# Optimization experiments

Measured on AMD Instinct MI355X. Metric: run time of the kernel, lower is better.

## Reference

```python
import jax, jax.numpy as jnp
import numpy as np

B, K, H, W = 8, 1024, 24, 24
C = H * W            # in_channels = 576
NH = 6               # hardcoded num_heads
HD = C // NH         # 96


def setup_inputs() -> dict:
    key = jax.random.key(0)
    ks = jax.random.split(key, 8)
    s = 1.0 / np.sqrt(C)
    return {
        "input1": jax.random.normal(ks[0], (B, K, H, W), jnp.float32),
        "input2": jax.random.normal(ks[1], (B, K, H, W), jnp.float32),
        "Wq": jax.random.uniform(ks[2], (C, C), jnp.float32, -s, s),
        "bq": jax.random.uniform(ks[3], (C,), jnp.float32, -s, s),
        "Wk": jax.random.uniform(ks[4], (C, C), jnp.float32, -s, s),
        "bk": jax.random.uniform(ks[5], (C,), jnp.float32, -s, s),
        "Wv": jax.random.uniform(ks[6], (C, C), jnp.float32, -s, s),
        "bv": jax.random.uniform(ks[7], (C,), jnp.float32, -s, s),
    }


def reference(input1, input2, Wq, bq, Wk, bk, Wv, bv):
    b, k, h, w = input1.shape
    c = h * w
    x1 = input1.reshape(b, k, c)
    x2 = input2.reshape(b, k, c)
    # torch nn.Linear: y = x @ W^T + b
    q = x1 @ Wq.T + bq                      # [b, k, c]
    kk = x2 @ Wk.T + bk
    v = x2 @ Wv.T + bv
    # torch .view scrambles: [b, k, c] -> [b, NH, c//NH, k] (row-major reshape)
    q = q.reshape(b, NH, c // NH, k)
    kk = kk.reshape(b, NH, c // NH, k)
    v = v.reshape(b, NH, c // NH, k)
    # scores = q^T k over head-dim; NOTE: no 1/sqrt(d) scaling in original
    scores = jnp.einsum('bhdq,bhdk->bhqk', q, kk)   # [b, NH, k, k]
    weights = jax.nn.softmax(scores, axis=-1)
    # context = value @ weights^T -> [b, NH, hd, k]
    ctx = jnp.einsum('bhdk,bhqk->bhdq', v, weights)
    return ctx.reshape(b, k, h, w)
```

## Files before the change

### kernel.cpp

```cpp
#include <hip/hip_runtime.h>
#include <cmath>

#define BATCH 8
#define KDIM  1024
#define CH    576
#define NHEAD 6
#define HDIM  96

typedef _Float16 f16;
typedef f16 f16x4 __attribute__((ext_vector_type(4)));
typedef f16 f16x8 __attribute__((ext_vector_type(8)));
typedef float f32x16 __attribute__((ext_vector_type(16)));
typedef unsigned int u32;

#define PSZ  (BATCH * KDIM * CH)
#define WSZ  (CH * CH)

__device__ inline f32x16 zero16() {
    f32x16 z;
#pragma unroll
    for (int r = 0; r < 16; ++r) z[r] = 0.f;
    return z;
}

__global__ __launch_bounds__(256) void convert_all(
    const float* __restrict__ x1, const float* __restrict__ x2,
    const float* __restrict__ Wq, const float* __restrict__ Wk,
    const float* __restrict__ Wv,
    f16* __restrict__ x1h, f16* __restrict__ x2h, f16* __restrict__ wh)
{
    const int bid = blockIdx.x;
    const int tid = threadIdx.x;

    __shared__ f16 Ws2[192 * 88];

    if (bid < 81) {
        const int z  = bid / 27;
        const int xb = (bid % 27) / 9;
        const int k0 = bid % 9;
        const float* src = (z == 0) ? Wq : (z == 1) ? Wk : Wv;

#pragma unroll
        for (int r = 0; r < 12; ++r) {
            int idx = r * 256 + tid;
            int row = idx >> 4, c4 = idx & 15;
            float4 u = *(const float4*)&src[(size_t)(xb * 192 + row) * CH + k0 * 64 + c4 * 4];
            f16x4 hv;
            hv[0] = (f16)u.x; hv[1] = (f16)u.y; hv[2] = (f16)u.z; hv[3] = (f16)u.w;
            *(f16x4*)&Ws2[row * 88 + c4 * 4] = hv;
        }
        __syncthreads();

        f16* dst = wh + ((size_t)((z * 3 + xb) * 9 + k0) * 24) * 512;
#pragma unroll
        for (int rr = 0; rr < 6; ++rr) {
            int cc = rr * 256 + tid;
            int lc = cc >> 6, lane = cc & 63;
            int ks = lc / 6, rem = lc % 6;
            int hw = rem / 3, nt = rem % 3;
            int n_local = hw * 96 + nt * 32 + (lane & 31);
            int kk = ks * 16 + (lane >> 5) * 8;
            f16x8 v = *(const f16x8*)&Ws2[n_local * 88 + kk];
            *(f16x8*)&dst[(size_t)cc * 8] = v;
        }
    } else {
        int idx = (bid - 81) * 256 + tid;
        const float* src;
        f16* dst;
        if (idx < PSZ / 8) { src = x1; dst = x1h; }
        else {
            idx -= PSZ / 8;
            if (idx >= PSZ / 8) return;
            src = x2; dst = x2h;
        }
        float4 u0 = ((const float4*)src)[2 * idx];
        float4 u1 = ((const float4*)src)[2 * idx + 1];
        f16x8 hv;
        hv[0] = (f16)u0.x; hv[1] = (f16)u0.y; hv[2] = (f16)u0.z; hv[3] = (f16)u0.w;
        hv[4] = (f16)u1.x; hv[5] = (f16)u1.y; hv[6] = (f16)u1.z; hv[7] = (f16)u1.w;
        ((f16x8*)dst)[idx] = hv;
    }
}

__global__ __launch_bounds__(256, 2) void proj_kernel(
    const f16* __restrict__ x1h, const f16* __restrict__ x2h,
    const f16* __restrict__ wh,
    const float* __restrict__ bq, const float* __restrict__ bk,
    const float* __restrict__ bv,
    f16* __restrict__ qf, f16* __restrict__ kf, f16* __restrict__ VF)
{
    const int bid = blockIdx.x;
    const int k8  = bid & 7;
    const int j   = bid >> 3;
    const int xb  = j % 3;
    const int z   = (j / 3) % 3;
    const int y   = k8 + 8 * (j / 9);

    const f16* A      = (z == 0) ? x1h : x2h;
    const float* bias = (z == 0) ? bq : (z == 1) ? bk : bv;

    __shared__ __align__(16) char sm[25600];
    f16* As = (f16*)sm;
    f16* Es = (f16*)sm;

    const int tid = threadIdx.x;
    const int lane = tid & 63, w = tid >> 6;
    const int l31 = lane & 31, half = lane >> 5;
    const int mw = 64 * (w & 1), nh = 96 * (w >> 1);
    const int nBase = xb * 192;
    const int mBase = y * 128;

    int arow[4], ach[4];
#pragma unroll
    for (int r = 0; r < 4; ++r) {
        int idx = r * 256 + tid;
        arow[r] = idx >> 3; ach[r] = idx & 7;
    }

    const f16* Wfrag = wh + ((size_t)(z * 3 + xb) * 216 + (size_t)(w >> 1) * 3) * 512
                          + (size_t)lane * 8;

    f16x8 aP[4];
#pragma unroll
    for (int r = 0; r < 4; ++r)
        aP[r] = *(const f16x8*)&A[(size_t)(mBase + arow[r]) * CH + ach[r] * 8];

    f16x8 wc[12];
#pragma unroll
    for (int ks = 0; ks < 4; ++ks)
#pragma unroll
        for (int nt = 0; nt < 3; ++nt)
            wc[ks * 3 + nt] = *(const f16x8*)&Wfrag[(size_t)(ks * 6 + nt) * 512];

    f32x16 acc[2][3] = {{zero16(), zero16(), zero16()},
                        {zero16(), zero16(), zero16()}};

    for (int k0i = 0; k0i < 9; ++k0i) {
        __syncthreads();
#pragma unroll
        for (int r = 0; r < 4; ++r)
            *(f16x8*)&As[arow[r] * 72 + ach[r] * 8] = aP[r];
        __syncthreads();
        if (k0i + 1 < 9) {
#pragma unroll
            for (int r = 0; r < 4; ++r)
                aP[r] = *(const f16x8*)&A[(size_t)(mBase + arow[r]) * CH + (k0i + 1) * 64 + ach[r] * 8];
        }
#pragma unroll
        for (int ks = 0; ks < 4; ++ks) {
            f16x8 a0 = *(const f16x8*)&As[(mw + l31) * 72 + 16 * ks + 8 * half];
            f16x8 a1 = *(const f16x8*)&As[(mw + 32 + l31) * 72 + 16 * ks + 8 * half];
#pragma unroll
            for (int nt = 0; nt < 3; ++nt) {
                acc[0][nt] = __builtin_amdgcn_mfma_f32_32x32x16_f16(a0, wc[ks * 3 + nt], acc[0][nt], 0, 0, 0);
                acc[1][nt] = __builtin_amdgcn_mfma_f32_32x32x16_f16(a1, wc[ks * 3 + nt], acc[1][nt], 0, 0, 0);
            }
        }
        if (k0i + 1 < 9) {
            const f16* Wn = Wfrag + (size_t)(k0i + 1) * 24 * 512;
#pragma unroll
            for (int ks = 0; ks < 4; ++ks)
#pragma unroll
                for (int nt = 0; nt < 3; ++nt)
                    wc[ks * 3 + nt] = *(const f16x8*)&Wn[(size_t)(ks * 6 + nt) * 512];
        }
    }

    if (z < 2) {
        f16* dst = (z == 0) ? qf : kf;
#pragma unroll
        for (int nt = 0; nt < 3; ++nt) {
            int n = nBase + nh + 32 * nt + l31;
            float bsv = bias[n];
#pragma unroll
            for (int ms = 0; ms < 2; ++ms)
#pragma unroll
                for (int r = 0; r < 16; ++r) {
                    int m = mBase + mw + 32 * ms + (r & 3) + 8 * (r >> 2) + 4 * half;
                    dst[(size_t)m * CH + n] = (f16)(acc[ms][nt][r] + bsv);
                }
        }
    } else {
        const int b      = y >> 3;
        const int kkBase = (y & 7) * 128;
#pragma unroll
        for (int hs = 0; hs < 2; ++hs) {
            __syncthreads();
            if ((w & 1) == hs) {
#pragma unroll
                for (int nt = 0; nt < 3; ++nt) {
                    int nloc = nh + 32 * nt + l31;
                    float bsv = bias[nBase + nloc];
#pragma unroll
                    for (int ms = 0; ms < 2; ++ms)
#pragma unroll
                        for (int r = 0; r < 16; ++r) {
                            int row_l = 32 * ms + (r & 3) + 8 * (r >> 2) + 4 * half;
                            Es[row_l * 200 + nloc] = (f16)(acc[ms][nt][r] + bsv);
                        }
                }
            }
            __syncthreads();
#pragma unroll
            for (int rr = 0; rr < 6; ++rr) {
                int o = rr * 256 + tid;
                int row_l = o / 24, sl = o % 24;
                int f = (kkBase + hs * 64 + row_l) * 576 + nBase + sl * 8;
                int h = f / 98304;
                int rem = f - h * 98304;
                int d = rem >> 10, t = rem & 1023;
                int tt2 = t >> 6, tl = t & 63;
                int c = (tl >> 5) * 384 + ((tl >> 4) & 1) * 192
                      + (d >> 5) * 64 + (d & 31) + 32 * ((tl >> 3) & 1);
                f16x8 v = *(const f16x8*)&Es[row_l * 200 + sl * 8];
                *(f16x8*)&VF[((size_t)((b * NHEAD + h) * 16 + tt2)) * 6144 + (size_t)c * 8] = v;
            }
        }
    }
}

__global__ __launch_bounds__(256) void repack_qk(
    const f16* __restrict__ qf, const f16* __restrict__ kf,
    f16* __restrict__ QF, f16* __restrict__ KF)
{
    const int tt = blockIdx.x;
    const int bh = blockIdx.y;
    const f16* src = blockIdx.z ? kf : qf;
    f16* dst = blockIdx.z ? KF : QF;
    const int tid = threadIdx.x;

    __shared__ f16 Ts[96 * 72];
    const int rowbase = (bh / NHEAD) * CH + (bh % NHEAD) * HDIM;

#pragma unroll
    for (int r = 0; r < 3; ++r) {
        int idx = r * 256 + tid;
        int d = idx >> 3, g = idx & 7;
        *(f16x8*)&Ts[d * 72 + g * 8] =
            *(const f16x8*)&src[(size_t)(rowbase + d) * KDIM + tt * 64 + g * 8];
    }
    __syncthreads();

    f16* dblk = dst + ((size_t)bh * 16 + tt) * 6144;
#pragma unroll
    for (int r = 0; r < 3; ++r) {
        int c = r * 256 + tid;
        int lane = c & 63;
        int ks = (c >> 6) % 6;
        int jg = c / 384;
        int l31 = lane & 31, half = lane >> 5;
        int jl = jg * 32 + l31;
        int d0 = ks * 16 + half * 8;
        f16x8 v;
#pragma unroll
        for (int u = 0; u < 8; ++u) v[u] = Ts[(d0 + u) * 72 + jl];
        *(f16x8*)&dblk[(size_t)c * 8] = v;
    }
}

__global__ __launch_bounds__(256, 3) void attn_kernel(
    const f16* __restrict__ QF, const f16* __restrict__ KF,
    const f16* __restrict__ VF, float* __restrict__ out)
{
    __shared__ __align__(16) char smem[25600];

    const int bh = blockIdx.x;
    const int qt = blockIdx.y;
    const int h  = bh % NHEAD;
    const int b  = bh / NHEAD;

    const int tid = threadIdx.x;
    const int lane = tid & 63, w = tid >> 6;
    const int ih = w & 1, jg = w >> 1;
    const int l31 = lane & 31, half = lane >> 5;
    const int iw = 32 * ih;

    const f16* Qblk  = QF + ((size_t)bh * 16 + qt) * 6144 + (size_t)ih * 3072 + (size_t)lane * 8;
    const f16* Kfrag = KF + (size_t)bh * 16 * 6144 + (size_t)jg * 3072 + (size_t)lane * 8;
    const f16* Vfrag = VF + (size_t)bh * 16 * 6144 + (size_t)jg * 3072 + (size_t)lane * 8;

    f16x8 qfr[6];
#pragma unroll
    for (int ks = 0; ks < 6; ++ks) {
        qfr[ks] = *(const f16x8*)&Qblk[ks * 512];
#pragma unroll
        for (int u = 0; u < 8; ++u)
            qfr[ks][u] = (f16)((float)qfr[ks][u] * 1.44269504f);
    }

    f16x8 kc[6], vc[6];
#pragma unroll
    for (int ks = 0; ks < 6; ++ks)
        kc[ks] = *(const f16x8*)&Kfrag[ks * 512];
#pragma unroll
    for (int kq = 0; kq < 2; ++kq)
#pragma unroll
        for (int t = 0; t < 3; ++t)
            vc[kq * 3 + t] = *(const f16x8*)&Vfrag[kq * 1536 + t * 512];

    float l_run = 0.f;
    f32x16 Oacc[3] = {zero16(), zero16(), zero16()};

    for (int jt = 0; jt < 16; ++jt) {
        f32x16 s0 = zero16();
#pragma unroll
        for (int ks = 0; ks < 6; ++ks)
            s0 = __builtin_amdgcn_mfma_f32_32x32x16_f16(kc[ks], qfr[ks], s0, 0, 0, 0);

        if (jt + 1 < 16) {
            const f16* Kt = Kfrag + (size_t)(jt + 1) * 6144;
#pragma unroll
            for (int ks = 0; ks < 6; ++ks)
                kc[ks] = *(const f16x8*)&Kt[ks * 512];
        }

        f16x4 pq[4];
#pragma unroll
        for (int r = 0; r < 16; ++r) {
            float e = __builtin_amdgcn_exp2f(s0[r] - 26.0f);
            l_run += e;
            pq[r >> 2][r & 3] = (f16)e;
        }

#pragma unroll
        for (int kq = 0; kq < 2; ++kq) {
            union { f16x4 h; u32 u[2]; } snd, rcv, keep;
            keep.h = half ? pq[2 * kq + 1] : pq[2 * kq];
            snd.h  = half ? pq[2 * kq]     : pq[2 * kq + 1];
            rcv.u[0] = __shfl_xor((int)snd.u[0], 32);
            rcv.u[1] = __shfl_xor((int)snd.u[1], 32);
            f16x8 bp;
            if (half == 0) {
#pragma unroll
                for (int v = 0; v < 4; ++v) { bp[v] = keep.h[v]; bp[4 + v] = rcv.h[v]; }
            } else {
#pragma unroll
                for (int v = 0; v < 4; ++v) { bp[v] = rcv.h[v]; bp[4 + v] = keep.h[v]; }
            }
#pragma unroll
            for (int t = 0; t < 3; ++t)
                Oacc[t] = __builtin_amdgcn_mfma_f32_32x32x16_f16(vc[kq * 3 + t], bp, Oacc[t], 0, 0, 0);
        }

        if (jt + 1 < 16) {
            const f16* Vt = Vfrag + (size_t)(jt + 1) * 6144;
#pragma unroll
            for (int kq = 0; kq < 2; ++kq)
#pragma unroll
                for (int t = 0; t < 3; ++t)
                    vc[kq * 3 + t] = *(const f16x8*)&Vt[kq * 1536 + t * 512];
        }
    }

    l_run += __shfl_xor(l_run, 32);

    float* Oscr = (float*)smem;
    float* lScr = (float*)(smem + 25344);
    if (jg == 1) {
        if (half == 0) lScr[iw + l31] = l_run;
        float* od = Oscr + ih * 3168;
#pragma unroll
        for (int t = 0; t < 3; ++t)
#pragma unroll
            for (int r = 0; r < 16; ++r) {
                int d = 32 * t + (r & 3) + 8 * (r >> 2) + 4 * half;
                od[d * 33 + l31] = Oacc[t][r];
            }
    }
    __syncthreads();
    if (jg == 0) {
        float linv = 1.0f / (l_run + lScr[iw + l31]);
        const float* od = Oscr + ih * 3168;
        float* obase = out + ((size_t)b * CH + (size_t)h * HDIM) * KDIM
                           + qt * 64 + iw + l31;
#pragma unroll
        for (int t = 0; t < 3; ++t)
#pragma unroll
            for (int r = 0; r < 16; ++r) {
                int d = 32 * t + (r & 3) + 8 * (r >> 2) + 4 * half;
                obase[(size_t)d * KDIM] =
                    (Oacc[t][r] + od[d * 33 + l31]) * linv;
            }
    }
}

extern "C" void kernel_launch(void* const* d_in, const int* in_sizes, int n_in,
                              void* d_out, int out_size, void* d_ws, size_t ws_size,
                              hipStream_t stream)
{
    const float* x1 = (const float*)d_in[0];
    const float* x2 = (const float*)d_in[1];
    const float* Wq = (const float*)d_in[2];
    const float* bq = (const float*)d_in[3];
    const float* Wk = (const float*)d_in[4];
    const float* bk = (const float*)d_in[5];
    const float* Wv = (const float*)d_in[6];
    const float* bv = (const float*)d_in[7];
    float* out = (float*)d_out;

    const size_t P = PSZ;
    f16* x1h = (f16*)d_ws;
    f16* x2h = x1h + P;
    f16* qf  = x2h + P;
    f16* kf  = qf + P;
    f16* QF  = kf + P;
    f16* KF  = QF + P;
    f16* VF  = KF + P;
    f16* wh  = VF + P;

    const int xblocks = 2 * (PSZ / 8) / 256;
    convert_all<<<81 + xblocks, 256, 0, stream>>>(x1, x2, Wq, Wk, Wv, x1h, x2h, wh);

    proj_kernel<<<576, 256, 0, stream>>>(x1h, x2h, wh, bq, bk, bv, qf, kf, VF);

    dim3 rgrid(KDIM / 64, BATCH * NHEAD, 2);
    repack_qk<<<rgrid, 256, 0, stream>>>(qf, kf, QF, KF);

    dim3 agrid(BATCH * NHEAD, KDIM / 64);
    attn_kernel<<<agrid, 256, 0, stream>>>(QF, KF, VF, out);
}
```

Baseline: 160.0 us.

## Fuse all stages into one persistent kernel with grid-wide atomic barriers

Replaces the four separate launches (convert, projection, repack, attention) with a single persistent kernel of 512 blocks. Each phase loops over virtual block indices, and phases are separated by a software grid barrier built on an atomic counter, which is reset by a memset before launch. The goal is to remove launch overhead and inter-kernel gaps. In exchange it adds spin-wait barriers, caps attention occupancy at the projection's launch bounds, and risks deadlock if all 512 blocks cannot be co-resident.

```diff
diff --git a/kernel.cpp b/kernel.cpp
--- a/kernel.cpp
+++ b/kernel.cpp
@@ -23,364 +23,372 @@
     return z;
 }
 
-__global__ __launch_bounds__(256) void convert_all(
-    const float* __restrict__ x1, const float* __restrict__ x2,
-    const float* __restrict__ Wq, const float* __restrict__ Wk,
-    const float* __restrict__ Wv,
-    f16* __restrict__ x1h, f16* __restrict__ x2h, f16* __restrict__ wh)
-{
-    const int bid = blockIdx.x;
-    const int tid = threadIdx.x;
-
-    __shared__ f16 Ws2[192 * 88];
-
-    if (bid < 81) {
-        const int z  = bid / 27;
-        const int xb = (bid % 27) / 9;
-        const int k0 = bid % 9;
-        const float* src = (z == 0) ? Wq : (z == 1) ? Wk : Wv;
-
-#pragma unroll
-        for (int r = 0; r < 12; ++r) {
-            int idx = r * 256 + tid;
-            int row = idx >> 4, c4 = idx & 15;
-            float4 u = *(const float4*)&src[(size_t)(xb * 192 + row) * CH + k0 * 64 + c4 * 4];
-            f16x4 hv;
-            hv[0] = (f16)u.x; hv[1] = (f16)u.y; hv[2] = (f16)u.z; hv[3] = (f16)u.w;
-            *(f16x4*)&Ws2[row * 88 + c4 * 4] = hv;
-        }
-        __syncthreads();
-
-        f16* dst = wh + ((size_t)((z * 3 + xb) * 9 + k0) * 24) * 512;
-#pragma unroll
-        for (int rr = 0; rr < 6; ++rr) {
-            int cc = rr * 256 + tid;
-            int lc = cc >> 6, lane = cc & 63;
-            int ks = lc / 6, rem = lc % 6;
-            int hw = rem / 3, nt = rem % 3;
-            int n_local = hw * 96 + nt * 32 + (lane & 31);
-            int kk = ks * 16 + (lane >> 5) * 8;
-            f16x8 v = *(const f16x8*)&Ws2[n_local * 88 + kk];
-            *(f16x8*)&dst[(size_t)cc * 8] = v;
-        }
-    } else {
-        int idx = (bid - 81) * 256 + tid;
-        const float* src;
-        f16* dst;
-        if (idx < PSZ / 8) { src = x1; dst = x1h; }
-        else {
-            idx -= PSZ / 8;
-            if (idx >= PSZ / 8) return;
-            src = x2; dst = x2h;
-        }
-        float4 u0 = ((const float4*)src)[2 * idx];
-        float4 u1 = ((const float4*)src)[2 * idx + 1];
-        f16x8 hv;
-        hv[0] = (f16)u0.x; hv[1] = (f16)u0.y; hv[2] = (f16)u0.z; hv[3] = (f16)u0.w;
-        hv[4] = (f16)u1.x; hv[5] = (f16)u1.y; hv[6] = (f16)u1.z; hv[7] = (f16)u1.w;
-        ((f16x8*)dst)[idx] = hv;
-    }
-}
-
-__global__ __launch_bounds__(256, 2) void proj_kernel(
-    const f16* __restrict__ x1h, const f16* __restrict__ x2h,
-    const f16* __restrict__ wh,
-    const float* __restrict__ bq, const float* __restrict__ bk,
-    const float* __restrict__ bv,
-    f16* __restrict__ qf, f16* __restrict__ kf, f16* __restrict__ VF)
-{
-    const int bid = blockIdx.x;
-    const int k8  = bid & 7;
-    const int j   = bid >> 3;
-    const int xb  = j % 3;
-    const int z   = (j / 3) % 3;
-    const int y   = k8 + 8 * (j / 9);
-
-    const f16* A      = (z == 0) ? x1h : x2h;
-    const float* bias = (z == 0) ? bq : (z == 1) ? bk : bv;
-
-    __shared__ __align__(16) char sm[25600];
-    f16* As = (f16*)sm;
-    f16* Es = (f16*)sm;
-
-    const int tid = threadIdx.x;
-    const int lane = tid & 63, w = tid >> 6;
-    const int l31 = lane & 31, half = lane >> 5;
-    const int mw = 64 * (w & 1), nh = 96 * (w >> 1);
-    const int nBase = xb * 192;
-    const int mBase = y * 128;
-
-    int arow[4], ach[4];
-#pragma unroll
-    for (int r = 0; r < 4; ++r) {
-        int idx = r * 256 + tid;
-        arow[r] = idx >> 3; ach[r] = idx & 7;
-    }
-
-    const f16* Wfrag = wh + ((size_t)(z * 3 + xb) * 216 + (size_t)(w >> 1) * 3) * 512
-                          + (size_t)lane * 8;
-
-    f16x8 aP[4];
-#pragma unroll
-    for (int r = 0; r < 4; ++r)
-        aP[r] = *(const f16x8*)&A[(size_t)(mBase + arow[r]) * CH + ach[r] * 8];
-
-    f16x8 wc[12];
-#pragma unroll
-    for (int ks = 0; ks < 4; ++ks)
-#pragma unroll
-        for (int nt = 0; nt < 3; ++nt)
-            wc[ks * 3 + nt] = *(const f16x8*)&Wfrag[(size_t)(ks * 6 + nt) * 512];
-
-    f32x16 acc[2][3] = {{zero16(), zero16(), zero16()},
-                        {zero16(), zero16(), zero16()}};
-
-    for (int k0i = 0; k0i < 9; ++k0i) {
-        __syncthreads();
-#pragma unroll
-        for (int r = 0; r < 4; ++r)
-            *(f16x8*)&As[arow[r] * 72 + ach[r] * 8] = aP[r];
-        __syncthreads();
-        if (k0i + 1 < 9) {
-#pragma unroll
-            for (int r = 0; r < 4; ++r)
-                aP[r] = *(const f16x8*)&A[(size_t)(mBase + arow[r]) * CH + (k0i + 1) * 64 + ach[r] * 8];
-        }
-#pragma unroll
-        for (int ks = 0; ks < 4; ++ks) {
-            f16x8 a0 = *(const f16x8*)&As[(mw + l31) * 72 + 16 * ks + 8 * half];
-            f16x8 a1 = *(const f16x8*)&As[(mw + 32 + l31) * 72 + 16 * ks + 8 * half];
-#pragma unroll
-            for (int nt = 0; nt < 3; ++nt) {
-                acc[0][nt] = __builtin_amdgcn_mfma_f32_32x32x16_f16(a0, wc[ks * 3 + nt], acc[0][nt], 0, 0, 0);
-                acc[1][nt] = __builtin_amdgcn_mfma_f32_32x32x16_f16(a1, wc[ks * 3 + nt], acc[1][nt], 0, 0, 0);
-            }
-        }
-        if (k0i + 1 < 9) {
-            const f16* Wn = Wfrag + (size_t)(k0i + 1) * 24 * 512;
-#pragma unroll
-            for (int ks = 0; ks < 4; ++ks)
-#pragma unroll
-                for (int nt = 0; nt < 3; ++nt)
-                    wc[ks * 3 + nt] = *(const f16x8*)&Wn[(size_t)(ks * 6 + nt) * 512];
-        }
-    }
-
-    if (z < 2) {
-        f16* dst = (z == 0) ? qf : kf;
-#pragma unroll
-        for (int nt = 0; nt < 3; ++nt) {
-            int n = nBase + nh + 32 * nt + l31;
-            float bsv = bias[n];
-#pragma unroll
-            for (int ms = 0; ms < 2; ++ms)
-#pragma unroll
-                for (int r = 0; r < 16; ++r) {
-                    int m = mBase + mw + 32 * ms + (r & 3) + 8 * (r >> 2) + 4 * half;
-                    dst[(size_t)m * CH + n] = (f16)(acc[ms][nt][r] + bsv);
-                }
-        }
-    } else {
-        const int b      = y >> 3;
-        const int kkBase = (y & 7) * 128;
-#pragma unroll
-        for (int hs = 0; hs < 2; ++hs) {
-            __syncthreads();
-            if ((w & 1) == hs) {
-#pragma unroll
-                for (int nt = 0; nt < 3; ++nt) {
-                    int nloc = nh + 32 * nt + l31;
-                    float bsv = bias[nBase + nloc];
-#pragma unroll
-                    for (int ms = 0; ms < 2; ++ms)
-#pragma unroll
-                        for (int r = 0; r < 16; ++r) {
-                            int row_l = 32 * ms + (r & 3) + 8 * (r >> 2) + 4 * half;
-                            Es[row_l * 200 + nloc] = (f16)(acc[ms][nt][r] + bsv);
-                        }
-                }
-            }
-            __syncthreads();
-#pragma unroll
-            for (int rr = 0; rr < 6; ++rr) {
-                int o = rr * 256 + tid;
-                int row_l = o / 24, sl = o % 24;
-                int f = (kkBase + hs * 64 + row_l) * 576 + nBase + sl * 8;
-                int h = f / 98304;
-                int rem = f - h * 98304;
-                int d = rem >> 10, t = rem & 1023;
-                int tt2 = t >> 6, tl = t & 63;
-                int c = (tl >> 5) * 384 + ((tl >> 4) & 1) * 192
-                      + (d >> 5) * 64 + (d & 31) + 32 * ((tl >> 3) & 1);
-                f16x8 v = *(const f16x8*)&Es[row_l * 200 + sl * 8];
-                *(f16x8*)&VF[((size_t)((b * NHEAD + h) * 16 + tt2)) * 6144 + (size_t)c * 8] = v;
-            }
-        }
-    }
-}
-
-__global__ __launch_bounds__(256) void repack_qk(
-    const f16* __restrict__ qf, const f16* __restrict__ kf,
-    f16* __restrict__ QF, f16* __restrict__ KF)
-{
-    const int tt = blockIdx.x;
-    const int bh = blockIdx.y;
-    const f16* src = blockIdx.z ? kf : qf;
-    f16* dst = blockIdx.z ? KF : QF;
-    const int tid = threadIdx.x;
-
-    __shared__ f16 Ts[96 * 72];
-    const int rowbase = (bh / NHEAD) * CH + (bh % NHEAD) * HDIM;
-
-#pragma unroll
-    for (int r = 0; r < 3; ++r) {
-        int idx = r * 256 + tid;
-        int d = idx >> 3, g = idx & 7;
-        *(f16x8*)&Ts[d * 72 + g * 8] =
-            *(const f16x8*)&src[(size_t)(rowbase + d) * KDIM + tt * 64 + g * 8];
+__device__ inline void gbar(u32* cnt, u32 target) {
+    __syncthreads();
+    if (threadIdx.x == 0) {
+        __threadfence();
+        atomicAdd(cnt, 1u);
+        while (atomicAdd(cnt, 0u) < target)
+            __builtin_amdgcn_s_sleep(2);
+        __threadfence();
     }
     __syncthreads();
-
-    f16* dblk = dst + ((size_t)bh * 16 + tt) * 6144;
-#pragma unroll
-    for (int r = 0; r < 3; ++r) {
-        int c = r * 256 + tid;
-        int lane = c & 63;
-        int ks = (c >> 6) % 6;
-        int jg = c / 384;
-        int l31 = lane & 31, half = lane >> 5;
-        int jl = jg * 32 + l31;
-        int d0 = ks * 16 + half * 8;
-        f16x8 v;
-#pragma unroll
-        for (int u = 0; u < 8; ++u) v[u] = Ts[(d0 + u) * 72 + jl];
-        *(f16x8*)&dblk[(size_t)c * 8] = v;
+}
+
+__global__ __launch_bounds__(256, 2) void mega_kernel(
+    const float* __restrict__ x1, const float* __restrict__ x2,
+    const float* __restrict__ Wq, const float* __restrict__ bq,
+    const float* __restrict__ Wk, const float* __restrict__ bk,
+    const float* __restrict__ Wv, const float* __restrict__ bv,
+    f16* __restrict__ x1h, f16* __restrict__ x2h,
+    f16* __restrict__ qf, f16* __restrict__ kf,
+    f16* __restrict__ QF, f16* __restrict__ KF, f16* __restrict__ VF,
+    f16* __restrict__ wh, u32* __restrict__ cnt, float* __restrict__ out)
+{
+    __shared__ __align__(16) char sm[33792];
+
+    const int tid = threadIdx.x;
+    const int nb  = gridDim.x;
+
+    for (int vb = blockIdx.x; vb < 81 + 2 * (PSZ / 8) / 256; vb += nb) {
+        if (vb < 81) {
+            f16* Ws2 = (f16*)sm;
+            const int z  = vb / 27;
+            const int xb = (vb % 27) / 9;
+            const int k0 = vb % 9;
+            const float* src = (z == 0) ? Wq : (z == 1) ? Wk : Wv;
+
+#pragma unroll
+            for (int r = 0; r < 12; ++r) {
+                int idx = r * 256 + tid;
+                int row = idx >> 4, c4 = idx & 15;
+                float4 u = *(const float4*)&src[(size_t)(xb * 192 + row) * CH + k0 * 64 + c4 * 4];
+                f16x4 hv;
+                hv[0] = (f16)u.x; hv[1] = (f16)u.y; hv[2] = (f16)u.z; hv[3] = (f16)u.w;
+                *(f16x4*)&Ws2[row * 88 + c4 * 4] = hv;
+            }
+            __syncthreads();
+
+            f16* dst = wh + ((size_t)((z * 3 + xb) * 9 + k0) * 24) * 512;
+#pragma unroll
+            for (int rr = 0; rr < 6; ++rr) {
+                int cc = rr * 256 + tid;
+                int lc = cc >> 6, lane = cc & 63;
+                int ks = lc / 6, rem = lc % 6;
+                int hw = rem / 3, nt = rem % 3;
+                int n_local = hw * 96 + nt * 32 + (lane & 31);
+                int kk = ks * 16 + (lane >> 5) * 8;
+                f16x8 v = *(const f16x8*)&Ws2[n_local * 88 + kk];
+                *(f16x8*)&dst[(size_t)cc * 8] = v;
+            }
+            __syncthreads();
+        } else {
+            int idx = (vb - 81) * 256 + tid;
+            const float* src;
+            f16* dst;
+            if (idx < PSZ / 8) { src = x1; dst = x1h; }
+            else {
+                idx -= PSZ / 8;
+                if (idx >= PSZ / 8) continue;
+                src = x2; dst = x2h;
+            }
+            float4 u0 = ((const float4*)src)[2 * idx];
+            float4 u1 = ((const float4*)src)[2 * idx + 1];
+            f16x8 hv;
+            hv[0] = (f16)u0.x; hv[1] = (f16)u0.y; hv[2] = (f16)u0.z; hv[3] = (f16)u0.w;
+            hv[4] = (f16)u1.x; hv[5] = (f16)u1.y; hv[6] = (f16)u1.z; hv[7] = (f16)u1.w;
+            ((f16x8*)dst)[idx] = hv;
+        }
     }
-}
-
-__global__ __launch_bounds__(256, 3) void attn_kernel(
-    const f16* __restrict__ QF, const f16* __restrict__ KF,
-    const f16* __restrict__ VF, float* __restrict__ out)
-{
-    __shared__ __align__(16) char smem[25600];
-
-    const int bh = blockIdx.x;
-    const int qt = blockIdx.y;
-    const int h  = bh % NHEAD;
-    const int b  = bh / NHEAD;
-
-    const int tid = threadIdx.x;
-    const int lane = tid & 63, w = tid >> 6;
-    const int ih = w & 1, jg = w >> 1;
-    const int l31 = lane & 31, half = lane >> 5;
-    const int iw = 32 * ih;
-
-    const f16* Qblk  = QF + ((size_t)bh * 16 + qt) * 6144 + (size_t)ih * 3072 + (size_t)lane * 8;
-    const f16* Kfrag = KF + (size_t)bh * 16 * 6144 + (size_t)jg * 3072 + (size_t)lane * 8;
-    const f16* Vfrag = VF + (size_t)bh * 16 * 6144 + (size_t)jg * 3072 + (size_t)lane * 8;
-
-    f16x8 qfr[6];
-#pragma unroll
-    for (int ks = 0; ks < 6; ++ks) {
-        qfr[ks] = *(const f16x8*)&Qblk[ks * 512];
-#pragma unroll
-        for (int u = 0; u < 8; ++u)
-            qfr[ks][u] = (f16)((float)qfr[ks][u] * 1.44269504f);
+    gbar(cnt, (u32)nb);
+
+    for (int vb = blockIdx.x; vb < 576; vb += nb) {
+        const int k8  = vb & 7;
+        const int j   = vb >> 3;
+        const int xb  = j % 3;
+        const int z   = (j / 3) % 3;
+        const int y   = k8 + 8 * (j / 9);
+
+        const f16* A      = (z == 0) ? x1h : x2h;
+        const float* bias = (z == 0) ? bq : (z == 1) ? bk : bv;
+
+        f16* As = (f16*)sm;
+        f16* Es = (f16*)sm;
+
+        const int lane = tid & 63, w = tid >> 6;
+        const int l31 = lane & 31, half = lane >> 5;
+        const int mw = 64 * (w & 1), nh = 96 * (w >> 1);
+        const int nBase = xb * 192;
+        const int mBase = y * 128;
+
+        int arow[4], ach[4];
+#pragma unroll
+        for (int r = 0; r < 4; ++r) {
+            int idx = r * 256 + tid;
+            arow[r] = idx >> 3; ach[r] = idx & 7;
+        }
+
+        const f16* Wfrag = wh + ((size_t)(z * 3 + xb) * 216 + (size_t)(w >> 1) * 3) * 512
+                              + (size_t)lane * 8;
+
+        f16x8 aP[4];
+#pragma unroll
+        for (int r = 0; r < 4; ++r)
+            aP[r] = *(const f16x8*)&A[(size_t)(mBase + arow[r]) * CH + ach[r] * 8];
+
+        f16x8 wc[12];
+#pragma unroll
+        for (int ks = 0; ks < 4; ++ks)
+#pragma unroll
+            for (int nt = 0; nt < 3; ++nt)
+                wc[ks * 3 + nt] = *(const f16x8*)&Wfrag[(size_t)(ks * 6 + nt) * 512];
+
+        f32x16 acc[2][3] = {{zero16(), zero16(), zero16()},
+                            {zero16(), zero16(), zero16()}};
+
+        for (int k0i = 0; k0i < 9; ++k0i) {
+            __syncthreads();
+#pragma unroll
+            for (int r = 0; r < 4; ++r)
+                *(f16x8*)&As[arow[r] * 72 + ach[r] * 8] = aP[r];
+            __syncthreads();
+            if (k0i + 1 < 9) {
+#pragma unroll
+                for (int r = 0; r < 4; ++r)
+                    aP[r] = *(const f16x8*)&A[(size_t)(mBase + arow[r]) * CH + (k0i + 1) * 64 + ach[r] * 8];
+            }
+#pragma unroll
+            for (int ks = 0; ks < 4; ++ks) {
+                f16x8 a0 = *(const f16x8*)&As[(mw + l31) * 72 + 16 * ks + 8 * half];
+                f16x8 a1 = *(const f16x8*)&As[(mw + 32 + l31) * 72 + 16 * ks + 8 * half];
+#pragma unroll
+                for (int nt = 0; nt < 3; ++nt) {
+                    acc[0][nt] = __builtin_amdgcn_mfma_f32_32x32x16_f16(a0, wc[ks * 3 + nt], acc[0][nt], 0, 0, 0);
+                    acc[1][nt] = __builtin_amdgcn_mfma_f32_32x32x16_f16(a1, wc[ks * 3 + nt], acc[1][nt], 0, 0, 0);
+                }
+            }
+            if (k0i + 1 < 9) {
+                const f16* Wn = Wfrag + (size_t)(k0i + 1) * 24 * 512;
+#pragma unroll
+                for (int ks = 0; ks < 4; ++ks)
+#pragma unroll
+                    for (int nt = 0; nt < 3; ++nt)
+                        wc[ks * 3 + nt] = *(const f16x8*)&Wn[(size_t)(ks * 6 + nt) * 512];
+            }
+        }
+
+        if (z < 2) {
+            f16* dst = (z == 0) ? qf : kf;
+#pragma unroll
+            for (int nt = 0; nt < 3; ++nt) {
+                int n = nBase + nh + 32 * nt + l31;
+                float bsv = bias[n];
+#pragma unroll
+                for (int ms = 0; ms < 2; ++ms)
+#pragma unroll
+                    for (int r = 0; r < 16; ++r) {
+                        int m = mBase + mw + 32 * ms + (r & 3) + 8 * (r >> 2) + 4 * half;
+                        dst[(size_t)m * CH + n] = (f16)(acc[ms][nt][r] + bsv);
+                    }
+            }
+        } else {
+            const int b      = y >> 3;
+            const int kkBase = (y & 7) * 128;
+#pragma unroll
+            for (int hs = 0; hs < 2; ++hs) {
+                __syncthreads();
+                if ((w & 1) == hs) {
+#pragma unroll
+                    for (int nt = 0; nt < 3; ++nt) {
+                        int nloc = nh + 32 * nt + l31;
+                        float bsv = bias[nBase + nloc];
+#pragma unroll
+                        for (int ms = 0; ms < 2; ++ms)
+#pragma unroll
+                            for (int r = 0; r < 16; ++r) {
+                                int row_l = 32 * ms + (r & 3) + 8 * (r >> 2) + 4 * half;
+                                Es[row_l * 200 + nloc] = (f16)(acc[ms][nt][r] + bsv);
+                            }
+                    }
+                }
+                __syncthreads();
+#pragma unroll
+                for (int rr = 0; rr < 6; ++rr) {
+                    int o = rr * 256 + tid;
+                    int row_l = o / 24, sl = o % 24;
+                    int f = (kkBase + hs * 64 + row_l) * 576 + nBase + sl * 8;
+                    int h = f / 98304;
+                    int rem = f - h * 98304;
+                    int d = rem >> 10, t = rem & 1023;
+                    int tt2 = t >> 6, tl = t & 1023 & 63;
+                    int c = (tl >> 5) * 384 + ((tl >> 4) & 1) * 192
+                          + (d >> 5) * 64 + (d & 31) + 32 * ((tl >> 3) & 1);
+                    f16x8 v = *(const f16x8*)&Es[row_l * 200 + sl * 8];
+                    *(f16x8*)&VF[((size_t)((b * NHEAD + h) * 16 + tt2)) * 6144 + (size_t)c * 8] = v;
+                }
+            }
+        }
+        __syncthreads();
     }
-
-    f16x8 kc[6], vc[6];
-#pragma unroll
-    for (int ks = 0; ks < 6; ++ks)
-        kc[ks] = *(const f16x8*)&Kfrag[ks * 512];
-#pragma unroll
-    for (int kq = 0; kq < 2; ++kq)
-#pragma unroll
-        for (int t = 0; t < 3; ++t)
-            vc[kq * 3 + t] = *(const f16x8*)&Vfrag[kq * 1536 + t * 512];
-
-    float l_run = 0.f;
-    f32x16 Oacc[3] = {zero16(), zero16(), zero16()};
-
-    for (int jt = 0; jt < 16; ++jt) {
-        f32x16 s0 = zero16();
+    gbar(cnt, 2u * (u32)nb);
+
+    for (int vb = blockIdx.x; vb < 1536; vb += nb) {
+        const int tt = vb & 15;
+        const int bh = (vb >> 4) % 48;
+        const int zz = vb / 768;
+        const f16* src = zz ? kf : qf;
+        f16* dst = zz ? KF : QF;
+
+        f16* Ts = (f16*)sm;
+        const int rowbase = (bh / NHEAD) * CH + (bh % NHEAD) * HDIM;
+
+#pragma unroll
+        for (int r = 0; r < 3; ++r) {
+            int idx = r * 256 + tid;
+            int d = idx >> 3, g = idx & 7;
+            *(f16x8*)&Ts[d * 72 + g * 8] =
+                *(const f16x8*)&src[(size_t)(rowbase + d) * KDIM + tt * 64 + g * 8];
+        }
+        __syncthreads();
+
+        f16* dblk = dst + ((size_t)bh * 16 + tt) * 6144;
+#pragma unroll
+        for (int r = 0; r < 3; ++r) {
+            int c = r * 256 + tid;
+            int lane = c & 63;
+            int ks = (c >> 6) % 6;
+            int jg = c / 384;
+            int l31 = lane & 31, half = lane >> 5;
+            int jl = jg * 32 + l31;
+            int d0 = ks * 16 + half * 8;
+            f16x8 v;
+#pragma unroll
+            for (int u = 0; u < 8; ++u) v[u] = Ts[(d0 + u) * 72 + jl];
+            *(f16x8*)&dblk[(size_t)c * 8] = v;
+        }
+        __syncthreads();
+    }
+    gbar(cnt, 3u * (u32)nb);
+
+    for (int vb = blockIdx.x; vb < 768; vb += nb) {
+        const int bh = vb % 48;
+        const int qt = vb / 48;
+        const int h  = bh % NHEAD;
+        const int b  = bh / NHEAD;
+
+        const int lane = tid & 63, w = tid >> 6;
+        const int ih = w & 1, jg = w >> 1;
+        const int l31 = lane & 31, half = lane >> 5;
+        const int iw = 32 * ih;
+
+        const f16* Qblk  = QF + ((size_t)bh * 16 + qt) * 6144 + (size_t)ih * 3072 + (size_t)lane * 8;
+        const f16* Kfrag = KF + (size_t)bh * 16 * 6144 + (size_t)jg * 3072 + (size_t)lane * 8;
+        const f16* Vfrag = VF + (size_t)bh * 16 * 6144 + (size_t)jg * 3072 + (size_t)lane * 8;
+
+        f16x8 qfr[6];
+#pragma unroll
+        for (int ks = 0; ks < 6; ++ks) {
+            qfr[ks] = *(const f16x8*)&Qblk[ks * 512];
+#pragma unroll
+            for (int u = 0; u < 8; ++u)
+                qfr[ks][u] = (f16)((float)qfr[ks][u] * 1.44269504f);
+        }
+
+        f16x8 kc[6], vc[6];
 #pragma unroll
         for (int ks = 0; ks < 6; ++ks)
-            s0 = __builtin_amdgcn_mfma_f32_32x32x16_f16(kc[ks], qfr[ks], s0, 0, 0, 0);
-
-        if (jt + 1 < 16) {
-            const f16* Kt = Kfrag + (size_t)(jt + 1) * 6144;
+            kc[ks] = *(const f16x8*)&Kfrag[ks * 512];
+#pragma unroll
+        for (int kq = 0; kq < 2; ++kq)
+#pragma unroll
+            for (int t = 0; t < 3; ++t)
+                vc[kq * 3 + t] = *(const f16x8*)&Vfrag[kq * 1536 + t * 512];
+
+        float l_run = 0.f;
+        f32x16 Oacc[3] = {zero16(), zero16(), zero16()};
+
+        for (int jt = 0; jt < 16; ++jt) {
+            f32x16 s0 = zero16();
 #pragma unroll
             for (int ks = 0; ks < 6; ++ks)
-                kc[ks] = *(const f16x8*)&Kt[ks * 512];
-        }
-
-        f16x4 pq[4];
-#pragma unroll
-        for (int r = 0; r < 16; ++r) {
-            float e = __builtin_amdgcn_exp2f(s0[r] - 26.0f);
-            l_run += e;
-            pq[r >> 2][r & 3] = (f16)e;
-        }
-
-#pragma unroll
-        for (int kq = 0; kq < 2; ++kq) {
-            union { f16x4 h; u32 u[2]; } snd, rcv, keep;
-            keep.h = half ? pq[2 * kq + 1] : pq[2 * kq];
-            snd.h  = half ? pq[2 * kq]     : pq[2 * kq + 1];
-            rcv.u[0] = __shfl_xor((int)snd.u[0], 32);
-            rcv.u[1] = __shfl_xor((int)snd.u[1], 32);
-            f16x8 bp;
-            if (half == 0) {
-#pragma unroll
-                for (int v = 0; v < 4; ++v) { bp[v] = keep.h[v]; bp[4 + v] = rcv.h[v]; }
-            } else {
-#pragma unroll
-                for (int v = 0; v < 4; ++v) { bp[v] = rcv.h[v]; bp[4 + v] = keep.h[v]; }
-            }
+                s0 = __builtin_amdgcn_mfma_f32_32x32x16_f16(kc[ks], qfr[ks], s0, 0, 0, 0);
+
+            if (jt + 1 < 16) {
+                const f16* Kt = Kfrag + (size_t)(jt + 1) * 6144;
+#pragma unroll
+                for (int ks = 0; ks < 6; ++ks)
+                    kc[ks] = *(const f16x8*)&Kt[ks * 512];
+            }
+
+            f16x4 pq[4];
+#pragma unroll
+            for (int r = 0; r < 16; ++r) {
+                float e = __builtin_amdgcn_exp2f(s0[r] - 26.0f);
+                l_run += e;
+                pq[r >> 2][r & 3] = (f16)e;
+            }
+
+#pragma unroll
+            for (int kq = 0; kq < 2; ++kq) {
+                union { f16x4 hh; u32 u[2]; } snd, rcv, keep;
+                keep.hh = half ? pq[2 * kq + 1] : pq[2 * kq];
+                snd.hh  = half ? pq[2 * kq]     : pq[2 * kq + 1];
+                rcv.u[0] = __shfl_xor((int)snd.u[0], 32);
+                rcv.u[1] = __shfl_xor((int)snd.u[1], 32);
+                f16x8 bp;
+                if (half == 0) {
+#pragma unroll
+                    for (int v = 0; v < 4; ++v) { bp[v] = keep.hh[v]; bp[4 + v] = rcv.hh[v]; }
+                } else {
+#pragma unroll
+                    for (int v = 0; v < 4; ++v) { bp[v] = rcv.hh[v]; bp[4 + v] = keep.hh[v]; }
+                }
+#pragma unroll
+                for (int t = 0; t < 3; ++t)
+                    Oacc[t] = __builtin_amdgcn_mfma_f32_32x32x16_f16(vc[kq * 3 + t], bp, Oacc[t], 0, 0, 0);
+            }
+
+            if (jt + 1 < 16) {
+                const f16* Vt = Vfrag + (size_t)(jt + 1) * 6144;
+#pragma unroll
+                for (int kq = 0; kq < 2; ++kq)
+#pragma unroll
+                    for (int t = 0; t < 3; ++t)
+                        vc[kq * 3 + t] = *(const f16x8*)&Vt[kq * 1536 + t * 512];
+            }
+        }
+
+        l_run += __shfl_xor(l_run, 32);
+
+        float* Oscr = (float*)sm;
+        float* lScr = (float*)(sm + 25344);
+        if (jg == 1) {
+            if (half == 0) lScr[iw + l31] = l_run;
+            float* od = Oscr + ih * 3168;
 #pragma unroll
             for (int t = 0; t < 3; ++t)
-                Oacc[t] = __builtin_amdgcn_mfma_f32_32x32x16_f16(vc[kq * 3 + t], bp, Oacc[t], 0, 0, 0);
-        }
-
-        if (jt + 1 < 16) {
-            const f16* Vt = Vfrag + (size_t)(jt + 1) * 6144;
-#pragma unroll
-            for (int kq = 0; kq < 2; ++kq)
-#pragma unroll
-                for (int t = 0; t < 3; ++t)
-                    vc[kq * 3 + t] = *(const f16x8*)&Vt[kq * 1536 + t * 512];
-        }
-    }
-
-    l_run += __shfl_xor(l_run, 32);
-
-    float* Oscr = (float*)smem;
-    float* lScr = (float*)(smem + 25344);
-    if (jg == 1) {
-        if (half == 0) lScr[iw + l31] = l_run;
-        float* od = Oscr + ih * 3168;
-#pragma unroll
-        for (int t = 0; t < 3; ++t)
-#pragma unroll
-            for (int r = 0; r < 16; ++r) {
-                int d = 32 * t + (r & 3) + 8 * (r >> 2) + 4 * half;
-                od[d * 33 + l31] = Oacc[t][r];
-            }
-    }
-    __syncthreads();
-    if (jg == 0) {
-        float linv = 1.0f / (l_run + lScr[iw + l31]);
-        const float* od = Oscr + ih * 3168;
-        float* obase = out + ((size_t)b * CH + (size_t)h * HDIM) * KDIM
-                           + qt * 64 + iw + l31;
-#pragma unroll
-        for (int t = 0; t < 3; ++t)
-#pragma unroll
-            for (int r = 0; r < 16; ++r) {
-                int d = 32 * t + (r & 3) + 8 * (r >> 2) + 4 * half;
-                obase[(size_t)d * KDIM] =
-                    (Oacc[t][r] + od[d * 33 + l31]) * linv;
-            }
+#pragma unroll
+                for (int r = 0; r < 16; ++r) {
+                    int d = 32 * t + (r & 3) + 8 * (r >> 2) + 4 * half;
+                    od[d * 33 + l31] = Oacc[t][r];
+                }
+        }
+        __syncthreads();
+        if (jg == 0) {
+            float linv = 1.0f / (l_run + lScr[iw + l31]);
+            const float* od = Oscr + ih * 3168;
+            float* obase = out + ((size_t)b * CH + (size_t)h * HDIM) * KDIM
+                               + qt * 64 + iw + l31;
+#pragma unroll
+            for (int t = 0; t < 3; ++t)
+#pragma unroll
+                for (int r = 0; r < 16; ++r) {
+                    int d = 32 * t + (r & 3) + 8 * (r >> 2) + 4 * half;
+                    obase[(size_t)d * KDIM] =
+                        (Oacc[t][r] + od[d * 33 + l31]) * linv;
+                }
+        }
+        __syncthreads();
     }
 }
 
@@ -407,15 +415,11 @@
     f16* KF  = QF + P;
     f16* VF  = KF + P;
     f16* wh  = VF + P;
-
-    const int xblocks = 2 * (PSZ / 8) / 256;
-    convert_all<<<81 + xblocks, 256, 0, stream>>>(x1, x2, Wq, Wk, Wv, x1h, x2h, wh);
-
-    proj_kernel<<<576, 256, 0, stream>>>(x1h, x2h, wh, bq, bk, bv, qf, kf, VF);
-
-    dim3 rgrid(KDIM / 64, BATCH * NHEAD, 2);
-    repack_qk<<<rgrid, 256, 0, stream>>>(qf, kf, QF, KF);
-
-    dim3 agrid(BATCH * NHEAD, KDIM / 64);
-    attn_kernel<<<agrid, 256, 0, stream>>>(QF, KF, VF, out);
+    u32* cnt = (u32*)(wh + 3 * WSZ);
+
+    hipMemsetAsync(cnt, 0, sizeof(u32), stream);
+
+    mega_kernel<<<512, 256, 0, stream>>>(
+        x1, x2, Wq, bq, Wk, bk, Wv, bv,
+        x1h, x2h, qf, kf, QF, KF, VF, wh, cnt, out);
 }
```

Result: slower. 334.9 us (+109.3%).
